# Kernel tuning notes

Hardware: AMD Instinct MI355X
Metric: run time of the kernel (lower is better)

## Reference

```python
import jax, jax.numpy as jnp
import numpy as np

B, T, D, H, C = 256, 512, 128, 256, 10


def gru_layer(x, Wih, Whh, bih, bhh):
    # x: [B,T,Din]; Wih: [3H,Din]; Whh: [3H,H]; biases: [3H]
    # PyTorch gate order: r, z, n
    gi = jnp.einsum('btd,gd->btg', x, Wih) + bih  # [B,T,3H] input part, precomputed
    gi = jnp.transpose(gi, (1, 0, 2))             # [T,B,3H] for scan

    def step(h, gi_t):
        gh = h @ Whh.T + bhh                      # [B,3H]
        r = jax.nn.sigmoid(gi_t[:, :H] + gh[:, :H])
        z = jax.nn.sigmoid(gi_t[:, H:2 * H] + gh[:, H:2 * H])
        n = jnp.tanh(gi_t[:, 2 * H:] + r * gh[:, 2 * H:])
        h_new = (1.0 - z) * n + z * h
        return h_new, h_new

    h0 = jnp.zeros((x.shape[0], H), dtype=x.dtype)
    _, hs = jax.lax.scan(step, h0, gi)            # hs: [T,B,H]
    return jnp.transpose(hs, (1, 0, 2))           # [B,T,H]


def setup_inputs() -> dict:
    key = jax.random.key(0)
    ks = jax.random.split(key, 12)
    s_in = 1.0 / np.sqrt(H)
    inp = {
        'x': jax.random.normal(ks[0], (B, T, D), dtype=jnp.float32),
        'Wih0': jax.random.uniform(ks[1], (3 * H, D), jnp.float32, -s_in, s_in),
        'Whh0': jax.random.uniform(ks[2], (3 * H, H), jnp.float32, -s_in, s_in),
        'bih0': jax.random.uniform(ks[3], (3 * H,), jnp.float32, -s_in, s_in),
        'bhh0': jax.random.uniform(ks[4], (3 * H,), jnp.float32, -s_in, s_in),
        'Wih1': jax.random.uniform(ks[5], (3 * H, H), jnp.float32, -s_in, s_in),
        'Whh1': jax.random.uniform(ks[6], (3 * H, H), jnp.float32, -s_in, s_in),
        'bih1': jax.random.uniform(ks[7], (3 * H,), jnp.float32, -s_in, s_in),
        'bhh1': jax.random.uniform(ks[8], (3 * H,), jnp.float32, -s_in, s_in),
        'Wfc': jax.random.uniform(ks[9], (C, H), jnp.float32, -s_in, s_in),
        'bfc': jax.random.uniform(ks[10], (C,), jnp.float32, -s_in, s_in),
    }
    return inp


def reference(x, Wih0, Whh0, bih0, bhh0, Wih1, Whh1, bih1, bhh1, Wfc, bfc):
    h1 = gru_layer(x, Wih0, Whh0, bih0, bhh0)     # [B,T,H]
    h2 = gru_layer(h1, Wih1, Whh1, bih1, bhh1)    # [B,T,H]
    last = h2[:, -1, :]                           # [B,H] last timestep
    return last @ Wfc.T + bfc                     # [B,C]
```

## Files before the change

kernel.cpp:

```cpp
#include <hip/hip_runtime.h>
#include <hip/hip_fp16.h>
#include <cstddef>
#include <cstdint>

#define B_  256
#define T_  512
#define D_  128
#define H_  256
#define G3_ 768
#define C_  10

typedef _Float16 f16x8 __attribute__((ext_vector_type(8)));
typedef float    f32x4 __attribute__((ext_vector_type(4)));

__device__ __forceinline__ float sigmoid_f(float x) {
    return 1.0f / (1.0f + __expf(-x));
}
__device__ __forceinline__ float tanh_f(float x) {
    return 1.0f - 2.0f / (__expf(2.0f * x) + 1.0f);
}

__device__ __forceinline__ unsigned int packh2(float a, float b) {
    unsigned short lo = __half_as_ushort(__float2half(a));
    unsigned short hi = __half_as_ushort(__float2half(b));
    return (unsigned int)lo | ((unsigned int)hi << 16);
}

__global__ void k_pack_whh(const float* __restrict__ Whh, uint4* __restrict__ Wl) {
    const int wnt = blockIdx.x;
    const int w  = wnt / 6;
    const int nt = wnt % 6;
    const int t  = threadIdx.x;
    const int kt = t >> 6;
    const int l  = t & 63;
    const int g  = nt >> 1;
    const int n  = g * 256 + w * 32 + (nt & 1) * 16 + (l & 15);
    const int k0 = kt * 32 + (l >> 4) * 8;
    const float* row = Whh + (size_t)n * H_ + k0;
    uint4 u;
    u.x = packh2(row[0], row[1]);
    u.y = packh2(row[2], row[3]);
    u.z = packh2(row[4], row[5]);
    u.w = packh2(row[6], row[7]);
    Wl[(size_t)wnt * 512 + t] = u;
}

__global__ void k_pack_wih(const float* __restrict__ W, uint4* __restrict__ Wp,
                           int K) {
    const int KT = K >> 5;
    const int f  = blockIdx.x * 4 + (threadIdx.x >> 6);
    const int l  = threadIdx.x & 63;
    const int ntile = f / KT;
    const int kt    = f - ntile * KT;
    const int n  = ntile * 16 + (l & 15);
    const int k0 = kt * 32 + (l >> 4) * 8;
    const float* row = W + (size_t)n * K + k0;
    uint4 u;
    u.x = packh2(row[0], row[1]);
    u.y = packh2(row[2], row[3]);
    u.z = packh2(row[4], row[5]);
    u.w = packh2(row[6], row[7]);
    Wp[(size_t)f * 64 + l] = u;
}

__global__ __launch_bounds__(256) void k_gemm_f16(
    const void* __restrict__ A, long Abstride, int tcShift, int aIsF16,
    const uint4* __restrict__ Wp,
    const float* __restrict__ bias, float* __restrict__ C,
    int K)
{
    const int tid = threadIdx.x;
    const int w  = tid >> 6;
    const int l  = tid & 63;
    const int c  = l & 15;
    const int g4 = l >> 4;
    const int m0 = blockIdx.y * 128;
    const int n0 = blockIdx.x * 128;
    const int KT = K >> 5;
    const int mask = (1 << tcShift) - 1;

    const int mg0 = m0 + w * 32 + c;
    const int mg1 = mg0 + 16;
    const size_t aoff0 = (size_t)(mg0 >> tcShift) * Abstride
                       + (size_t)(mg0 & mask) * K + g4 * 8;
    const size_t aoff1 = (size_t)(mg1 >> tcShift) * Abstride
                       + (size_t)(mg1 & mask) * K + g4 * 8;
    const float*    Af0 = (const float*)A    + aoff0;
    const float*    Af1 = (const float*)A    + aoff1;
    const _Float16* Ah0 = (const _Float16*)A + aoff0;
    const _Float16* Ah1 = (const _Float16*)A + aoff1;

    const uint4* Wb = Wp + (size_t)((n0 >> 4) * KT) * 64 + l;

    f32x4 acc[2][8] = {};

    for (int kt = 0; kt < KT; kt++) {
        f16x8 a0, a1;
        if (aIsF16) {
            a0 = *(const f16x8*)(Ah0 + kt * 32);
            a1 = *(const f16x8*)(Ah1 + kt * 32);
        } else {
            float4 lo = *(const float4*)(Af0 + kt * 32);
            float4 hi = *(const float4*)(Af0 + kt * 32 + 4);
            a0[0] = (_Float16)lo.x; a0[1] = (_Float16)lo.y;
            a0[2] = (_Float16)lo.z; a0[3] = (_Float16)lo.w;
            a0[4] = (_Float16)hi.x; a0[5] = (_Float16)hi.y;
            a0[6] = (_Float16)hi.z; a0[7] = (_Float16)hi.w;
            lo = *(const float4*)(Af1 + kt * 32);
            hi = *(const float4*)(Af1 + kt * 32 + 4);
            a1[0] = (_Float16)lo.x; a1[1] = (_Float16)lo.y;
            a1[2] = (_Float16)lo.z; a1[3] = (_Float16)lo.w;
            a1[4] = (_Float16)hi.x; a1[5] = (_Float16)hi.y;
            a1[6] = (_Float16)hi.z; a1[7] = (_Float16)hi.w;
        }
#pragma unroll
        for (int ct = 0; ct < 8; ct++) {
            uint4 wf = Wb[(size_t)(ct * KT + kt) * 64];
            acc[0][ct] = __builtin_amdgcn_mfma_f32_16x16x32_f16(
                a0, __builtin_bit_cast(f16x8, wf), acc[0][ct], 0, 0, 0);
            acc[1][ct] = __builtin_amdgcn_mfma_f32_16x16x32_f16(
                a1, __builtin_bit_cast(f16x8, wf), acc[1][ct], 0, 0, 0);
        }
    }

#pragma unroll
    for (int ct = 0; ct < 8; ct++) {
        const int n = n0 + ct * 16 + c;
        const float bv = bias[n];
#pragma unroll
        for (int rt = 0; rt < 2; rt++) {
#pragma unroll
            for (int rg = 0; rg < 4; rg++) {
                const int m = m0 + w * 32 + rt * 16 + g4 * 4 + rg;
                C[(size_t)m * G3_ + n] = acc[rt][ct][rg] + bv;
            }
        }
    }
}

__device__ __forceinline__ void gru_scan_core(
    const float* __restrict__ gi,
    const uint4* __restrict__ Wpk,
    const float* __restrict__ bhh,
    float* __restrict__ h_state,
    _Float16* __restrict__ out_seq,
    int Tc, int initZero,
    uint4 (&lds_w)[8192], _Float16 (&lds_h)[2][16][264])
{
    const int tid = threadIdx.x;
    const int w  = tid >> 6;
    const int l  = tid & 63;
    const int c  = l & 15;
    const int g4 = l >> 4;

#pragma unroll
    for (int i = 0; i < 16; i++) {
        int idx = i * 512 + tid;
        lds_w[idx] = Wpk[(size_t)(idx >> 10) * 3072 + 2048 + (idx & 1023)];
    }

    uint4 wreg[32];
#pragma unroll
    for (int nt = 0; nt < 4; nt++)
#pragma unroll
        for (int kt = 0; kt < 8; kt++)
            wreg[nt * 8 + kt] = Wpk[(size_t)((w * 6 + nt) * 8 + kt) * 64 + l];

    const int jA = w * 32 + c;
    const float br0 = bhh[jA],       br1 = bhh[jA + 16];
    const float bz0 = bhh[256 + jA], bz1 = bhh[256 + jA + 16];
    const float bn0 = bhh[512 + jA], bn1 = bhh[512 + jA + 16];

    float hreg[4][2];
#pragma unroll
    for (int r = 0; r < 4; r++) {
        const int m = g4 * 4 + r;
        if (initZero) {
            hreg[r][0] = 0.0f;
            hreg[r][1] = 0.0f;
        } else {
            hreg[r][0] = h_state[(size_t)m * H_ + jA];
            hreg[r][1] = h_state[(size_t)m * H_ + jA + 16];
        }
        lds_h[0][m][jA]      = (_Float16)hreg[r][0];
        lds_h[0][m][jA + 16] = (_Float16)hreg[r][1];
    }
    __syncthreads();

    int cur = 0;
    for (int tt = 0; tt < Tc; ++tt) {
        unsigned wb = (unsigned)(w * 1024 + l);
        asm volatile("" : "+v"(wb));

        float gic[4][6];
#pragma unroll
        for (int r = 0; r < 4; r++) {
            const float* gp = gi + ((size_t)(g4 * 4 + r) * Tc + tt) * G3_ + jA;
#pragma unroll
            for (int gg = 0; gg < 3; gg++) {
                gic[r][gg * 2 + 0] = gp[gg * 256];
                gic[r][gg * 2 + 1] = gp[gg * 256 + 16];
            }
        }

        f32x4 acc[6] = {};
#pragma unroll
        for (int kt = 0; kt < 8; kt++) {
            f16x8 a = *(const f16x8*)&lds_h[cur][c][kt * 32 + g4 * 8];
#pragma unroll
            for (int nt = 0; nt < 4; nt++)
                acc[nt] = __builtin_amdgcn_mfma_f32_16x16x32_f16(
                    a, __builtin_bit_cast(f16x8, wreg[nt * 8 + kt]), acc[nt], 0, 0, 0);
            uint4 u4 = lds_w[wb + kt * 64];
            acc[4] = __builtin_amdgcn_mfma_f32_16x16x32_f16(
                a, __builtin_bit_cast(f16x8, u4), acc[4], 0, 0, 0);
            uint4 u5 = lds_w[wb + (8 + kt) * 64];
            acc[5] = __builtin_amdgcn_mfma_f32_16x16x32_f16(
                a, __builtin_bit_cast(f16x8, u5), acc[5], 0, 0, 0);
        }

#pragma unroll
        for (int r = 0; r < 4; r++) {
            const int m = g4 * 4 + r;
#pragma unroll
            for (int jj = 0; jj < 2; jj++) {
                float rg = sigmoid_f(gic[r][jj]     + acc[jj][r]     + (jj ? br1 : br0));
                float zg = sigmoid_f(gic[r][2 + jj] + acc[2 + jj][r] + (jj ? bz1 : bz0));
                float ng = tanh_f(gic[r][4 + jj] +
                                  rg * (acc[4 + jj][r] + (jj ? bn1 : bn0)));
                float hn = (1.0f - zg) * ng + zg * hreg[r][jj];
                hreg[r][jj] = hn;
                _Float16 hq = (_Float16)hn;
                lds_h[cur ^ 1][m][jA + jj * 16] = hq;
                if (out_seq)
                    out_seq[((size_t)m * Tc + tt) * H_ + jA + jj * 16] = hq;
            }
        }
        if (tt == Tc - 1) {
#pragma unroll
            for (int r = 0; r < 4; r++) {
                const int m = g4 * 4 + r;
                h_state[(size_t)m * H_ + jA]      = hreg[r][0];
                h_state[(size_t)m * H_ + jA + 16] = hreg[r][1];
            }
        }
        __syncthreads();
        cur ^= 1;
    }
}

__global__ __launch_bounds__(512, 2) void k_gru_scan_fused(
    const float* __restrict__ gi0, const uint4* __restrict__ wl0,
    const float* __restrict__ bhh0, float* __restrict__ hst0,
    _Float16* __restrict__ h1c,
    const float* __restrict__ gi1, const uint4* __restrict__ wl1,
    const float* __restrict__ bhh1, float* __restrict__ hst1,
    int Tc, int do0, int do1, int init0, int init1)
{
    __shared__ __align__(16) uint4    lds_w[8192];
    __shared__ __align__(16) _Float16 lds_h[2][16][264];

    const int blk = blockIdx.x;
    if (blk < 16) {
        if (!do0) return;
        const int b0 = blk * 16;
        gru_scan_core(gi0 + (size_t)b0 * Tc * G3_, wl0, bhh0,
                      hst0 + (size_t)b0 * H_, h1c + (size_t)b0 * Tc * H_,
                      Tc, init0, lds_w, lds_h);
    } else {
        if (!do1) return;
        const int b0 = (blk - 16) * 16;
        gru_scan_core(gi1 + (size_t)b0 * Tc * G3_, wl1, bhh1,
                      hst1 + (size_t)b0 * H_, nullptr,
                      Tc, init1, lds_w, lds_h);
    }
}

__global__ void k_fc(const float* __restrict__ h, const float* __restrict__ Wfc,
                     const float* __restrict__ bfc, float* __restrict__ out)
{
    int idx = blockIdx.x * blockDim.x + threadIdx.x;
    if (idx >= B_ * C_) return;
    int b = idx / C_, c = idx % C_;
    const float* hp = h + (size_t)b * H_;
    const float* wp = Wfc + (size_t)c * H_;
    float s = bfc[c];
#pragma unroll 4
    for (int k = 0; k < H_; k++) s = fmaf(hp[k], wp[k], s);
    out[idx] = s;
}

extern "C" void kernel_launch(void* const* d_in, const int* in_sizes, int n_in,
                              void* d_out, int out_size, void* d_ws, size_t ws_size,
                              hipStream_t stream)
{
    const float* x    = (const float*)d_in[0];
    const float* Wih0 = (const float*)d_in[1];
    const float* Whh0 = (const float*)d_in[2];
    const float* bih0 = (const float*)d_in[3];
    const float* bhh0 = (const float*)d_in[4];
    const float* Wih1 = (const float*)d_in[5];
    const float* Whh1 = (const float*)d_in[6];
    const float* bih1 = (const float*)d_in[7];
    const float* bhh1 = (const float*)d_in[8];
    const float* Wfc  = (const float*)d_in[9];
    const float* bfc  = (const float*)d_in[10];
    float* out = (float*)d_out;

    const size_t wlBytes  = (size_t)48 * 512 * sizeof(uint4);
    const size_t wp0Bytes = (size_t)48 * 4 * 64 * sizeof(uint4);
    const size_t wp1Bytes = (size_t)48 * 8 * 64 * sizeof(uint4);

    const size_t fixedB = 2 * wlBytes + wp0Bytes + wp1Bytes
                        + 2 * (size_t)B_ * H_ * 4 + 16384;
    int Tc = 64, tcShift = 6;
    while (Tc > 1) {
        size_t need = fixedB
                    + 2 * (size_t)B_ * Tc * G3_ * 4
                    + (size_t)B_ * Tc * H_ * 2;
        if (need <= ws_size) break;
        Tc >>= 1; tcShift--;
    }
    const int nChunks = T_ / Tc;

    char* ws = (char*)d_ws;
    size_t off = 0;
    auto alloc = [&](size_t bytes) { char* p = ws + off; off += (bytes + 255) & ~(size_t)255; return p; };
    float*    gi0 = (float*)alloc((size_t)B_ * Tc * G3_ * 4);
    float*    gi1 = (float*)alloc((size_t)B_ * Tc * G3_ * 4);
    _Float16* h1c = (_Float16*)alloc((size_t)B_ * Tc * H_ * 2);
    uint4* wl0  = (uint4*)alloc(wlBytes);
    uint4* wl1  = (uint4*)alloc(wlBytes);
    uint4* wp0  = (uint4*)alloc(wp0Bytes);
    uint4* wp1  = (uint4*)alloc(wp1Bytes);
    float* hst0 = (float*)alloc((size_t)B_ * H_ * 4);
    float* hst1 = (float*)alloc((size_t)B_ * H_ * 4);

    k_pack_whh<<<48, 512, 0, stream>>>(Whh0, wl0);
    k_pack_whh<<<48, 512, 0, stream>>>(Whh1, wl1);
    k_pack_wih<<<48, 256, 0, stream>>>(Wih0, wp0, D_);
    k_pack_wih<<<96, 256, 0, stream>>>(Wih1, wp1, H_);

    const dim3 ggrid(G3_ / 128, (B_ * Tc) / 128);

    k_gemm_f16<<<ggrid, 256, 0, stream>>>(
        x, (long)T_ * D_, tcShift, 0, wp0, bih0, gi0, D_);
    k_gru_scan_fused<<<32, 512, 0, stream>>>(
        gi0, wl0, bhh0, hst0, h1c, gi1, wl1, bhh1, hst1,
        Tc, 1, 0, 1, 0);

    for (int c = 1; c < nChunks; ++c) {
        k_gemm_f16<<<ggrid, 256, 0, stream>>>(
            h1c, (long)Tc * H_, tcShift, 1, wp1, bih1, gi1, H_);
        k_gemm_f16<<<ggrid, 256, 0, stream>>>(
            x + (size_t)c * Tc * D_, (long)T_ * D_, tcShift, 0, wp0, bih0, gi0, D_);
        k_gru_scan_fused<<<32, 512, 0, stream>>>(
            gi0, wl0, bhh0, hst0, h1c, gi1, wl1, bhh1, hst1,
            Tc, 1, 1, 0, c == 1);
    }

    k_gemm_f16<<<ggrid, 256, 0, stream>>>(
        h1c, (long)Tc * H_, tcShift, 1, wp1, bih1, gi1, H_);
    k_gru_scan_fused<<<32, 512, 0, stream>>>(
        gi0, wl0, bhh0, hst0, h1c, gi1, wl1, bhh1, hst1,
        Tc, 0, 1, 0, nChunks == 1);

    k_fc<<<10, 256, 0, stream>>>(hst1, Wfc, bfc, out);
}
```

Measured before the change: 2.155 ms.

## Overlap next-chunk layer-0 input GEMM with scan via extra blocks

Adds extra workgroups to the fused scan kernel that compute the next chunk's layer-0 input projection into a double-buffered gi0 buffer while the 32 scan blocks run. This removes one separate GEMM launch per chunk from the serial launch chain and puts idle CUs to work during the latency-bound scan. It costs an extra gi0 buffer, which may shrink Tc if workspace is tight, and the GEMM blocks share the kernel's large LDS and launch-bounds footprint.

```diff
diff --git a/kernel.cpp b/kernel.cpp
--- a/kernel.cpp
+++ b/kernel.cpp
@@ -255,7 +255,10 @@
     _Float16* __restrict__ h1c,
     const float* __restrict__ gi1, const uint4* __restrict__ wl1,
     const float* __restrict__ bhh1, float* __restrict__ hst1,
-    int Tc, int do0, int do1, int init0, int init1)
+    int Tc, int do0, int do1, int init0, int init1,
+    const float* __restrict__ gx, const uint4* __restrict__ wp0,
+    const float* __restrict__ bih0, float* __restrict__ gi0n,
+    int doGemm, int tcShift)
 {
     __shared__ __align__(16) uint4    lds_w[8192];
     __shared__ __align__(16) _Float16 lds_h[2][16][264];
@@ -267,12 +270,72 @@
         gru_scan_core(gi0 + (size_t)b0 * Tc * G3_, wl0, bhh0,
                       hst0 + (size_t)b0 * H_, h1c + (size_t)b0 * Tc * H_,
                       Tc, init0, lds_w, lds_h);
-    } else {
+    } else if (blk < 32) {
         if (!do1) return;
         const int b0 = (blk - 16) * 16;
         gru_scan_core(gi1 + (size_t)b0 * Tc * G3_, wl1, bhh1,
                       hst1 + (size_t)b0 * H_, nullptr,
                       Tc, init1, lds_w, lds_h);
+    } else {
+        if (!doGemm) return;
+        const int gb = blk - 32;
+        const int tid = threadIdx.x;
+        const int w  = tid >> 6;
+        const int l  = tid & 63;
+        const int c  = l & 15;
+        const int g4 = l >> 4;
+        const int n0 = (gb % 6) * 128;
+        const int m0 = (gb / 6) * 256 + w * 32;
+        const int mask = (1 << tcShift) - 1;
+
+        const int mg0 = m0 + c;
+        const int mg1 = mg0 + 16;
+        const float* Af0 = gx + (size_t)(mg0 >> tcShift) * (T_ * D_)
+                              + (size_t)(mg0 & mask) * D_ + g4 * 8;
+        const float* Af1 = gx + (size_t)(mg1 >> tcShift) * (T_ * D_)
+                              + (size_t)(mg1 & mask) * D_ + g4 * 8;
+        const uint4* Wb = wp0 + (size_t)((n0 >> 4) * 4) * 64 + l;
+
+        f32x4 acc[2][8] = {};
+#pragma unroll
+        for (int kt = 0; kt < 4; kt++) {
+            f16x8 a0, a1;
+            {
+                float4 lo = *(const float4*)(Af0 + kt * 32);
+                float4 hi = *(const float4*)(Af0 + kt * 32 + 4);
+                a0[0] = (_Float16)lo.x; a0[1] = (_Float16)lo.y;
+                a0[2] = (_Float16)lo.z; a0[3] = (_Float16)lo.w;
+                a0[4] = (_Float16)hi.x; a0[5] = (_Float16)hi.y;
+                a0[6] = (_Float16)hi.z; a0[7] = (_Float16)hi.w;
+                lo = *(const float4*)(Af1 + kt * 32);
+                hi = *(const float4*)(Af1 + kt * 32 + 4);
+                a1[0] = (_Float16)lo.x; a1[1] = (_Float16)lo.y;
+                a1[2] = (_Float16)lo.z; a1[3] = (_Float16)lo.w;
+                a1[4] = (_Float16)hi.x; a1[5] = (_Float16)hi.y;
+                a1[6] = (_Float16)hi.z; a1[7] = (_Float16)hi.w;
+            }
+#pragma unroll
+            for (int ct = 0; ct < 8; ct++) {
+                uint4 wf = Wb[(size_t)(ct * 4 + kt) * 64];
+                acc[0][ct] = __builtin_amdgcn_mfma_f32_16x16x32_f16(
+                    a0, __builtin_bit_cast(f16x8, wf), acc[0][ct], 0, 0, 0);
+                acc[1][ct] = __builtin_amdgcn_mfma_f32_16x16x32_f16(
+                    a1, __builtin_bit_cast(f16x8, wf), acc[1][ct], 0, 0, 0);
+            }
+        }
+#pragma unroll
+        for (int ct = 0; ct < 8; ct++) {
+            const int n = n0 + ct * 16 + c;
+            const float bv = bih0[n];
+#pragma unroll
+            for (int rt = 0; rt < 2; rt++) {
+#pragma unroll
+                for (int rg = 0; rg < 4; rg++) {
+                    const int m = m0 + rt * 16 + g4 * 4 + rg;
+                    gi0n[(size_t)m * G3_ + n] = acc[rt][ct][rg] + bv;
+                }
+            }
+        }
     }
 }
 
@@ -316,7 +379,7 @@
     int Tc = 64, tcShift = 6;
     while (Tc > 1) {
         size_t need = fixedB
-                    + 2 * (size_t)B_ * Tc * G3_ * 4
+                    + 3 * (size_t)B_ * Tc * G3_ * 4
                     + (size_t)B_ * Tc * H_ * 2;
         if (need <= ws_size) break;
         Tc >>= 1; tcShift--;
@@ -326,9 +389,10 @@
     char* ws = (char*)d_ws;
     size_t off = 0;
     auto alloc = [&](size_t bytes) { char* p = ws + off; off += (bytes + 255) & ~(size_t)255; return p; };
-    float*    gi0 = (float*)alloc((size_t)B_ * Tc * G3_ * 4);
-    float*    gi1 = (float*)alloc((size_t)B_ * Tc * G3_ * 4);
-    _Float16* h1c = (_Float16*)alloc((size_t)B_ * Tc * H_ * 2);
+    float*    gi0a = (float*)alloc((size_t)B_ * Tc * G3_ * 4);
+    float*    gi0b = (float*)alloc((size_t)B_ * Tc * G3_ * 4);
+    float*    gi1  = (float*)alloc((size_t)B_ * Tc * G3_ * 4);
+    _Float16* h1c  = (_Float16*)alloc((size_t)B_ * Tc * H_ * 2);
     uint4* wl0  = (uint4*)alloc(wlBytes);
     uint4* wl1  = (uint4*)alloc(wlBytes);
     uint4* wp0  = (uint4*)alloc(wp0Bytes);
@@ -336,34 +400,39 @@
     float* hst0 = (float*)alloc((size_t)B_ * H_ * 4);
     float* hst1 = (float*)alloc((size_t)B_ * H_ * 4);
 
+    float* gi0buf[2] = { gi0a, gi0b };
+
     k_pack_whh<<<48, 512, 0, stream>>>(Whh0, wl0);
     k_pack_whh<<<48, 512, 0, stream>>>(Whh1, wl1);
     k_pack_wih<<<48, 256, 0, stream>>>(Wih0, wp0, D_);
     k_pack_wih<<<96, 256, 0, stream>>>(Wih1, wp1, H_);
 
     const dim3 ggrid(G3_ / 128, (B_ * Tc) / 128);
+    const int NG = 32 + 6 * ((B_ * Tc) / 256);
 
     k_gemm_f16<<<ggrid, 256, 0, stream>>>(
-        x, (long)T_ * D_, tcShift, 0, wp0, bih0, gi0, D_);
-    k_gru_scan_fused<<<32, 512, 0, stream>>>(
-        gi0, wl0, bhh0, hst0, h1c, gi1, wl1, bhh1, hst1,
-        Tc, 1, 0, 1, 0);
+        x, (long)T_ * D_, tcShift, 0, wp0, bih0, gi0buf[0], D_);
+    k_gru_scan_fused<<<NG, 512, 0, stream>>>(
+        gi0buf[0], wl0, bhh0, hst0, h1c, gi1, wl1, bhh1, hst1,
+        Tc, 1, 0, 1, 0,
+        x + (size_t)1 * Tc * D_, wp0, bih0, gi0buf[1], nChunks > 1, tcShift);
 
     for (int c = 1; c < nChunks; ++c) {
         k_gemm_f16<<<ggrid, 256, 0, stream>>>(
             h1c, (long)Tc * H_, tcShift, 1, wp1, bih1, gi1, H_);
-        k_gemm_f16<<<ggrid, 256, 0, stream>>>(
-            x + (size_t)c * Tc * D_, (long)T_ * D_, tcShift, 0, wp0, bih0, gi0, D_);
-        k_gru_scan_fused<<<32, 512, 0, stream>>>(
-            gi0, wl0, bhh0, hst0, h1c, gi1, wl1, bhh1, hst1,
-            Tc, 1, 1, 0, c == 1);
+        k_gru_scan_fused<<<NG, 512, 0, stream>>>(
+            gi0buf[c & 1], wl0, bhh0, hst0, h1c, gi1, wl1, bhh1, hst1,
+            Tc, 1, 1, 0, c == 1,
+            x + (size_t)(c + 1) * Tc * D_, wp0, bih0, gi0buf[(c + 1) & 1],
+            c + 1 < nChunks, tcShift);
     }
 
     k_gemm_f16<<<ggrid, 256, 0, stream>>>(
         h1c, (long)Tc * H_, tcShift, 1, wp1, bih1, gi1, H_);
-    k_gru_scan_fused<<<32, 512, 0, stream>>>(
-        gi0, wl0, bhh0, hst0, h1c, gi1, wl1, bhh1, hst1,
-        Tc, 0, 1, 0, nChunks == 1);
+    k_gru_scan_fused<<<NG, 512, 0, stream>>>(
+        gi0buf[0], wl0, bhh0, hst0, h1c, gi1, wl1, bhh1, hst1,
+        Tc, 0, 1, 0, nChunks == 1,
+        x, wp0, bih0, gi0buf[1], 0, tcShift);
 
     k_fc<<<10, 256, 0, stream>>>(hst1, Wfc, bfc, out);
 }
```

Result: faster. 1.997 ms (-7.3%).

## Replace per-chunk launches with persistent kernel using flag-based producer/consumer pipelining

Applied to the files above, without the earlier changes.

Merges the per-chunk GEMM and scan launches into one persistent kernel. 32 blocks run the two GRU layer scans and 224 blocks compute the input-projection GEMMs. They coordinate through global atomic counters, and the gi and h1 buffers are double-buffered, so the GEMM for the next chunk overlaps the current scan. This removes launch overhead and the serialization between the GEMM and scan stages, and lets layer 0 and layer 1 run concurrently across chunks. The cost is spin-waiting and the need for all 256 blocks to be co-resident, or the waits deadlock and then exit through the bounded spin guard.

```diff
diff --git a/kernel.cpp b/kernel.cpp
--- a/kernel.cpp
+++ b/kernel.cpp
@@ -24,6 +24,23 @@
     unsigned short lo = __half_as_ushort(__float2half(a));
     unsigned short hi = __half_as_ushort(__float2half(b));
     return (unsigned int)lo | ((unsigned int)hi << 16);
+}
+
+__device__ __forceinline__ void block_wait(int* flag, int target) {
+    if (threadIdx.x == 0) {
+        int grd = 0;
+        while (__hip_atomic_load(flag, __ATOMIC_ACQUIRE,
+                                 __HIP_MEMORY_SCOPE_AGENT) < target &&
+               ++grd < (1 << 22)) {}
+    }
+    __syncthreads();
+}
+__device__ __forceinline__ void block_post(int* flag) {
+    __threadfence();
+    __syncthreads();
+    if (threadIdx.x == 0)
+        __hip_atomic_fetch_add(flag, 1, __ATOMIC_RELEASE,
+                               __HIP_MEMORY_SCOPE_AGENT);
 }
 
 __global__ void k_pack_whh(const float* __restrict__ Whh, uint4* __restrict__ Wl) {
@@ -63,23 +80,21 @@
     Wp[(size_t)f * 64 + l] = u;
 }
 
-__global__ __launch_bounds__(256) void k_gemm_f16(
+__device__ void gemm_unit(
     const void* __restrict__ A, long Abstride, int tcShift, int aIsF16,
-    const uint4* __restrict__ Wp,
-    const float* __restrict__ bias, float* __restrict__ C,
-    int K)
+    const uint4* __restrict__ Wp, const float* __restrict__ bias,
+    float* __restrict__ C, int K, int v, int n0)
 {
     const int tid = threadIdx.x;
     const int w  = tid >> 6;
     const int l  = tid & 63;
     const int c  = l & 15;
     const int g4 = l >> 4;
-    const int m0 = blockIdx.y * 128;
-    const int n0 = blockIdx.x * 128;
+    const int m0 = v * 256 + w * 32;
     const int KT = K >> 5;
     const int mask = (1 << tcShift) - 1;
 
-    const int mg0 = m0 + w * 32 + c;
+    const int mg0 = m0 + c;
     const int mg1 = mg0 + 16;
     const size_t aoff0 = (size_t)(mg0 >> tcShift) * Abstride
                        + (size_t)(mg0 & mask) * K + g4 * 8;
@@ -131,20 +146,21 @@
         for (int rt = 0; rt < 2; rt++) {
 #pragma unroll
             for (int rg = 0; rg < 4; rg++) {
-                const int m = m0 + w * 32 + rt * 16 + g4 * 4 + rg;
+                const int m = m0 + rt * 16 + g4 * 4 + rg;
                 C[(size_t)m * G3_ + n] = acc[rt][ct][rg] + bv;
             }
         }
     }
 }
 
-__device__ __forceinline__ void gru_scan_core(
-    const float* __restrict__ gi,
-    const uint4* __restrict__ Wpk,
-    const float* __restrict__ bhh,
-    float* __restrict__ h_state,
-    _Float16* __restrict__ out_seq,
-    int Tc, int initZero,
+__device__ void scan_role(
+    int isL0, int b0,
+    const float* __restrict__ giA, const float* __restrict__ giB,
+    const uint4* __restrict__ Wpk, const float* __restrict__ bhh,
+    _Float16* __restrict__ h1cA, _Float16* __restrict__ h1cB,
+    float* __restrict__ hstFinal,
+    int Tc, int nChunks, int UPC,
+    int* C0, int* C1, int* G0, int* G1,
     uint4 (&lds_w)[8192], _Float16 (&lds_h)[2][16][264])
 {
     const int tid = threadIdx.x;
@@ -175,104 +191,154 @@
 #pragma unroll
     for (int r = 0; r < 4; r++) {
         const int m = g4 * 4 + r;
-        if (initZero) {
-            hreg[r][0] = 0.0f;
-            hreg[r][1] = 0.0f;
+        hreg[r][0] = 0.0f;
+        hreg[r][1] = 0.0f;
+        lds_h[0][m][jA]      = (_Float16)0.0f;
+        lds_h[0][m][jA + 16] = (_Float16)0.0f;
+    }
+    __syncthreads();
+
+    int cur = 0;
+    for (int ck = 0; ck < nChunks; ++ck) {
+        if (isL0) {
+            block_wait(G0, UPC * (ck + 1));
+            if (ck >= 2) block_wait(G1, UPC * (ck - 1));
         } else {
-            hreg[r][0] = h_state[(size_t)m * H_ + jA];
-            hreg[r][1] = h_state[(size_t)m * H_ + jA + 16];
-        }
-        lds_h[0][m][jA]      = (_Float16)hreg[r][0];
-        lds_h[0][m][jA + 16] = (_Float16)hreg[r][1];
-    }
-    __syncthreads();
-
-    int cur = 0;
-    for (int tt = 0; tt < Tc; ++tt) {
-        unsigned wb = (unsigned)(w * 1024 + l);
-        asm volatile("" : "+v"(wb));
-
-        float gic[4][6];
-#pragma unroll
-        for (int r = 0; r < 4; r++) {
-            const float* gp = gi + ((size_t)(g4 * 4 + r) * Tc + tt) * G3_ + jA;
-#pragma unroll
-            for (int gg = 0; gg < 3; gg++) {
-                gic[r][gg * 2 + 0] = gp[gg * 256];
-                gic[r][gg * 2 + 1] = gp[gg * 256 + 16];
+            block_wait(G1, UPC * (ck + 1));
+        }
+        const float* gi = ((ck & 1) ? giB : giA) + (size_t)b0 * Tc * G3_;
+        _Float16* oseq = isL0
+            ? ((ck & 1) ? h1cB : h1cA) + (size_t)b0 * Tc * H_ : nullptr;
+
+        for (int tt = 0; tt < Tc; ++tt) {
+            unsigned wb = (unsigned)(w * 1024 + l);
+            asm volatile("" : "+v"(wb));
+
+            float gic[4][6];
+#pragma unroll
+            for (int r = 0; r < 4; r++) {
+                const float* gp = gi + ((size_t)(g4 * 4 + r) * Tc + tt) * G3_ + jA;
+#pragma unroll
+                for (int gg = 0; gg < 3; gg++) {
+                    gic[r][gg * 2 + 0] = gp[gg * 256];
+                    gic[r][gg * 2 + 1] = gp[gg * 256 + 16];
+                }
             }
-        }
-
-        f32x4 acc[6] = {};
-#pragma unroll
-        for (int kt = 0; kt < 8; kt++) {
-            f16x8 a = *(const f16x8*)&lds_h[cur][c][kt * 32 + g4 * 8];
-#pragma unroll
-            for (int nt = 0; nt < 4; nt++)
-                acc[nt] = __builtin_amdgcn_mfma_f32_16x16x32_f16(
-                    a, __builtin_bit_cast(f16x8, wreg[nt * 8 + kt]), acc[nt], 0, 0, 0);
-            uint4 u4 = lds_w[wb + kt * 64];
-            acc[4] = __builtin_amdgcn_mfma_f32_16x16x32_f16(
-                a, __builtin_bit_cast(f16x8, u4), acc[4], 0, 0, 0);
-            uint4 u5 = lds_w[wb + (8 + kt) * 64];
-            acc[5] = __builtin_amdgcn_mfma_f32_16x16x32_f16(
-                a, __builtin_bit_cast(f16x8, u5), acc[5], 0, 0, 0);
-        }
-
+
+            f32x4 acc[6] = {};
+#pragma unroll
+            for (int kt = 0; kt < 8; kt++) {
+                f16x8 a = *(const f16x8*)&lds_h[cur][c][kt * 32 + g4 * 8];
+#pragma unroll
+                for (int nt = 0; nt < 4; nt++)
+                    acc[nt] = __builtin_amdgcn_mfma_f32_16x16x32_f16(
+                        a, __builtin_bit_cast(f16x8, wreg[nt * 8 + kt]), acc[nt], 0, 0, 0);
+                uint4 u4 = lds_w[wb + kt * 64];
+                acc[4] = __builtin_amdgcn_mfma_f32_16x16x32_f16(
+                    a, __builtin_bit_cast(f16x8, u4), acc[4], 0, 0, 0);
+                uint4 u5 = lds_w[wb + (8 + kt) * 64];
+                acc[5] = __builtin_amdgcn_mfma_f32_16x16x32_f16(
+                    a, __builtin_bit_cast(f16x8, u5), acc[5], 0, 0, 0);
+            }
+
+#pragma unroll
+            for (int r = 0; r < 4; r++) {
+                const int m = g4 * 4 + r;
+#pragma unroll
+                for (int jj = 0; jj < 2; jj++) {
+                    float rg = sigmoid_f(gic[r][jj]     + acc[jj][r]     + (jj ? br1 : br0));
+                    float zg = sigmoid_f(gic[r][2 + jj] + acc[2 + jj][r] + (jj ? bz1 : bz0));
+                    float ng = tanh_f(gic[r][4 + jj] +
+                                      rg * (acc[4 + jj][r] + (jj ? bn1 : bn0)));
+                    float hn = (1.0f - zg) * ng + zg * hreg[r][jj];
+                    hreg[r][jj] = hn;
+                    _Float16 hq = (_Float16)hn;
+                    lds_h[cur ^ 1][m][jA + jj * 16] = hq;
+                    if (oseq)
+                        oseq[((size_t)m * Tc + tt) * H_ + jA + jj * 16] = hq;
+                }
+            }
+            __syncthreads();
+            cur ^= 1;
+        }
+        block_post(isL0 ? C0 : C1);
+    }
+
+    if (!isL0) {
+        float* hp = hstFinal + (size_t)b0 * H_;
 #pragma unroll
         for (int r = 0; r < 4; r++) {
             const int m = g4 * 4 + r;
-#pragma unroll
-            for (int jj = 0; jj < 2; jj++) {
-                float rg = sigmoid_f(gic[r][jj]     + acc[jj][r]     + (jj ? br1 : br0));
-                float zg = sigmoid_f(gic[r][2 + jj] + acc[2 + jj][r] + (jj ? bz1 : bz0));
-                float ng = tanh_f(gic[r][4 + jj] +
-                                  rg * (acc[4 + jj][r] + (jj ? bn1 : bn0)));
-                float hn = (1.0f - zg) * ng + zg * hreg[r][jj];
-                hreg[r][jj] = hn;
-                _Float16 hq = (_Float16)hn;
-                lds_h[cur ^ 1][m][jA + jj * 16] = hq;
-                if (out_seq)
-                    out_seq[((size_t)m * Tc + tt) * H_ + jA + jj * 16] = hq;
-            }
-        }
-        if (tt == Tc - 1) {
-#pragma unroll
-            for (int r = 0; r < 4; r++) {
-                const int m = g4 * 4 + r;
-                h_state[(size_t)m * H_ + jA]      = hreg[r][0];
-                h_state[(size_t)m * H_ + jA + 16] = hreg[r][1];
-            }
-        }
-        __syncthreads();
-        cur ^= 1;
-    }
-}
-
-__global__ __launch_bounds__(512, 2) void k_gru_scan_fused(
-    const float* __restrict__ gi0, const uint4* __restrict__ wl0,
-    const float* __restrict__ bhh0, float* __restrict__ hst0,
-    _Float16* __restrict__ h1c,
-    const float* __restrict__ gi1, const uint4* __restrict__ wl1,
-    const float* __restrict__ bhh1, float* __restrict__ hst1,
-    int Tc, int do0, int do1, int init0, int init1)
+            hp[(size_t)m * H_ + jA]      = hreg[r][0];
+            hp[(size_t)m * H_ + jA + 16] = hreg[r][1];
+        }
+    }
+}
+
+__global__ __launch_bounds__(512, 2) void k_gru_persist(
+    const float* __restrict__ x,
+    const uint4* __restrict__ wl0, const uint4* __restrict__ wl1,
+    const uint4* __restrict__ wp0, const uint4* __restrict__ wp1,
+    const float* __restrict__ bih0, const float* __restrict__ bih1,
+    const float* __restrict__ bhh0, const float* __restrict__ bhh1,
+    float* __restrict__ gi0A, float* __restrict__ gi0B,
+    float* __restrict__ gi1A, float* __restrict__ gi1B,
+    _Float16* __restrict__ h1cA, _Float16* __restrict__ h1cB,
+    float* __restrict__ hst1, int* __restrict__ flags,
+    int Tc, int tcShift, int nChunks)
 {
     __shared__ __align__(16) uint4    lds_w[8192];
     __shared__ __align__(16) _Float16 lds_h[2][16][264];
 
+    int* C0 = flags;
+    int* C1 = flags + 16;
+    int* G0 = flags + 32;
+    int* G1 = flags + 48;
+    const int UPC = (B_ * Tc / 256) * 6;
+
     const int blk = blockIdx.x;
     if (blk < 16) {
-        if (!do0) return;
-        const int b0 = blk * 16;
-        gru_scan_core(gi0 + (size_t)b0 * Tc * G3_, wl0, bhh0,
-                      hst0 + (size_t)b0 * H_, h1c + (size_t)b0 * Tc * H_,
-                      Tc, init0, lds_w, lds_h);
+        scan_role(1, blk * 16, gi0A, gi0B, wl0, bhh0, h1cA, h1cB, nullptr,
+                  Tc, nChunks, UPC, C0, C1, G0, G1, lds_w, lds_h);
+    } else if (blk < 32) {
+        scan_role(0, (blk - 16) * 16, gi1A, gi1B, wl1, bhh1, nullptr, nullptr,
+                  hst1, Tc, nChunks, UPC, C0, C1, G0, G1, lds_w, lds_h);
     } else {
-        if (!do1) return;
-        const int b0 = (blk - 16) * 16;
-        gru_scan_core(gi1 + (size_t)b0 * Tc * G3_, wl1, bhh1,
-                      hst1 + (size_t)b0 * H_, nullptr,
-                      Tc, init1, lds_w, lds_h);
+        const int q = blk - 32;
+        for (int p = 0; p <= nChunks; ++p) {
+            if (p == 0) {
+                for (int u = q; u < UPC; u += 224) {
+                    gemm_unit(x, (long)T_ * D_, tcShift, 0, wp0, bih0,
+                              gi0A, D_, u / 6, (u % 6) * 128);
+                    block_post(G0);
+                }
+                if (nChunks > 1)
+                    for (int u = q; u < UPC; u += 224) {
+                        gemm_unit(x + (size_t)Tc * D_, (long)T_ * D_, tcShift,
+                                  0, wp0, bih0, gi0B, D_, u / 6, (u % 6) * 128);
+                        block_post(G0);
+                    }
+            } else {
+                block_wait(C0, 16 * p);
+                if (p >= 3) block_wait(C1, 16 * (p - 2));
+                const _Float16* hsrc = ((p - 1) & 1) ? h1cB : h1cA;
+                float* g1dst = ((p - 1) & 1) ? gi1B : gi1A;
+                for (int u = q; u < UPC; u += 224) {
+                    gemm_unit(hsrc, (long)Tc * H_, tcShift, 1, wp1, bih1,
+                              g1dst, H_, u / 6, (u % 6) * 128);
+                    block_post(G1);
+                }
+                if (p + 1 <= nChunks - 1) {
+                    float* g0dst = ((p + 1) & 1) ? gi0B : gi0A;
+                    const float* xsrc = x + (size_t)(p + 1) * Tc * D_;
+                    for (int u = q; u < UPC; u += 224) {
+                        gemm_unit(xsrc, (long)T_ * D_, tcShift, 0, wp0, bih0,
+                                  g0dst, D_, u / 6, (u % 6) * 128);
+                        block_post(G0);
+                    }
+                }
+            }
+        }
     }
 }
 
@@ -310,14 +376,15 @@
     const size_t wlBytes  = (size_t)48 * 512 * sizeof(uint4);
     const size_t wp0Bytes = (size_t)48 * 4 * 64 * sizeof(uint4);
     const size_t wp1Bytes = (size_t)48 * 8 * 64 * sizeof(uint4);
-
-    const size_t fixedB = 2 * wlBytes + wp0Bytes + wp1Bytes
-                        + 2 * (size_t)B_ * H_ * 4 + 16384;
+    const size_t flBytes  = 64 * sizeof(int);
+
+    const size_t fixedB = 2 * wlBytes + wp0Bytes + wp1Bytes + flBytes
+                        + (size_t)B_ * H_ * 4 + 16384;
     int Tc = 64, tcShift = 6;
     while (Tc > 1) {
         size_t need = fixedB
-                    + 2 * (size_t)B_ * Tc * G3_ * 4
-                    + (size_t)B_ * Tc * H_ * 2;
+                    + 4 * (size_t)B_ * Tc * G3_ * 4
+                    + 2 * (size_t)B_ * Tc * H_ * 2;
         if (need <= ws_size) break;
         Tc >>= 1; tcShift--;
     }
@@ -326,44 +393,30 @@
     char* ws = (char*)d_ws;
     size_t off = 0;
     auto alloc = [&](size_t bytes) { char* p = ws + off; off += (bytes + 255) & ~(size_t)255; return p; };
-    float*    gi0 = (float*)alloc((size_t)B_ * Tc * G3_ * 4);
-    float*    gi1 = (float*)alloc((size_t)B_ * Tc * G3_ * 4);
-    _Float16* h1c = (_Float16*)alloc((size_t)B_ * Tc * H_ * 2);
+    float*    gi0A = (float*)alloc((size_t)B_ * Tc * G3_ * 4);
+    float*    gi0B = (float*)alloc((size_t)B_ * Tc * G3_ * 4);
+    float*    gi1A = (float*)alloc((size_t)B_ * Tc * G3_ * 4);
+    float*    gi1B = (float*)alloc((size_t)B_ * Tc * G3_ * 4);
+    _Float16* h1cA = (_Float16*)alloc((size_t)B_ * Tc * H_ * 2);
+    _Float16* h1cB = (_Float16*)alloc((size_t)B_ * Tc * H_ * 2);
     uint4* wl0  = (uint4*)alloc(wlBytes);
     uint4* wl1  = (uint4*)alloc(wlBytes);
     uint4* wp0  = (uint4*)alloc(wp0Bytes);
     uint4* wp1  = (uint4*)alloc(wp1Bytes);
-    float* hst0 = (float*)alloc((size_t)B_ * H_ * 4);
     float* hst1 = (float*)alloc((size_t)B_ * H_ * 4);
+    int*   flags = (int*)alloc(flBytes);
+
+    hipMemsetAsync(flags, 0, flBytes, stream);
 
     k_pack_whh<<<48, 512, 0, stream>>>(Whh0, wl0);
     k_pack_whh<<<48, 512, 0, stream>>>(Whh1, wl1);
     k_pack_wih<<<48, 256, 0, stream>>>(Wih0, wp0, D_);
     k_pack_wih<<<96, 256, 0, stream>>>(Wih1, wp1, H_);
 
-    const dim3 ggrid(G3_ / 128, (B_ * Tc) / 128);
-
-    k_gemm_f16<<<ggrid, 256, 0, stream>>>(
-        x, (long)T_ * D_, tcShift, 0, wp0, bih0, gi0, D_);
-    k_gru_scan_fused<<<32, 512, 0, stream>>>(
-        gi0, wl0, bhh0, hst0, h1c, gi1, wl1, bhh1, hst1,
-        Tc, 1, 0, 1, 0);
-
-    for (int c = 1; c < nChunks; ++c) {
-        k_gemm_f16<<<ggrid, 256, 0, stream>>>(
-            h1c, (long)Tc * H_, tcShift, 1, wp1, bih1, gi1, H_);
-        k_gemm_f16<<<ggrid, 256, 0, stream>>>(
-            x + (size_t)c * Tc * D_, (long)T_ * D_, tcShift, 0, wp0, bih0, gi0, D_);
-        k_gru_scan_fused<<<32, 512, 0, stream>>>(
-            gi0, wl0, bhh0, hst0, h1c, gi1, wl1, bhh1, hst1,
-            Tc, 1, 1, 0, c == 1);
-    }
-
-    k_gemm_f16<<<ggrid, 256, 0, stream>>>(
-        h1c, (long)Tc * H_, tcShift, 1, wp1, bih1, gi1, H_);
-    k_gru_scan_fused<<<32, 512, 0, stream>>>(
-        gi0, wl0, bhh0, hst0, h1c, gi1, wl1, bhh1, hst1,
-        Tc, 0, 1, 0, nChunks == 1);
+    k_gru_persist<<<256, 512, 0, stream>>>(
+        x, wl0, wl1, wp0, wp1, bih0, bih1, bhh0, bhh1,
+        gi0A, gi0B, gi1A, gi1B, h1cA, h1cB, hst1, flags,
+        Tc, tcShift, nChunks);
 
     k_fc<<<10, 256, 0, stream>>>(hst1, Wfc, bfc, out);
 }
```

Measured after the change: 5.522 ms. 2.56x slower.
